# Kernel tuning notes

Hardware: AMD Instinct MI355X
Metric: run time of the kernel (lower is better)

Reference implementation:

```python
import jax, jax.numpy as jnp
import numpy as np

N, E, D, T = 100000, 1600000, 128, 5
EPS = 1e-5


def setup_inputs() -> dict:
    key = jax.random.key(0)
    ks = jax.random.split(key, 8)
    scale = 1.0 / np.sqrt(D)
    return {
        "features": jax.random.normal(ks[0], (N, D), dtype=jnp.float32),
        "src": jax.random.randint(ks[1], (E,), 0, N, dtype=jnp.int32),
        "dst": jax.random.randint(ks[2], (E,), 0, N, dtype=jnp.int32),
        "etype": jax.random.randint(ks[3], (E,), 0, T, dtype=jnp.int32),
        "w1": jax.random.normal(ks[4], (T * D, D), dtype=jnp.float32) * scale,
        "b1": jnp.zeros((T * D,), dtype=jnp.float32),
        "g1": jnp.ones((D,), dtype=jnp.float32),
        "be1": jnp.zeros((D,), dtype=jnp.float32),
        "w2": jax.random.normal(ks[5], (T * D, D), dtype=jnp.float32) * scale,
        "b2": jnp.zeros((T * D,), dtype=jnp.float32),
        "g2": jnp.ones((D,), dtype=jnp.float32),
        "be2": jnp.zeros((D,), dtype=jnp.float32),
    }


def _bn(x, gamma, beta):
    # BatchNorm1d in training mode: biased batch statistics over node axis.
    mu = jnp.mean(x, axis=0)
    var = jnp.mean((x - mu) ** 2, axis=0)
    return gamma * (x - mu) * jax.lax.rsqrt(var + EPS) + beta


def _round(x, w, b, gamma, beta, src, dst, etype):
    h = jax.nn.relu(_bn(x, gamma, beta))
    h = jnp.einsum('nd,od->no', h, w) + b          # [N, T*D]
    h3 = h.reshape(N, T, D)
    # one-hot multiply + sum over types == select the etype slice per edge
    msg = h3[src, etype]                            # [E, D] gather
    return jax.ops.segment_sum(msg, dst, num_segments=N)  # [N, D] scatter-add


def reference(features, src, dst, etype, w1, b1, g1, be1, w2, b2, g2, be2):
    h_new = _round(features, w1, b1, g1, be1, src, dst, etype)
    h_new = _round(h_new, w2, b2, g2, be2, src, dst, etype)
    return h_new + features
```

## Files before the change

### kernel.cpp

```cpp
#include <hip/hip_runtime.h>

#define NN 100000
#define EE 1600000
#define DD 128
#define TD 640
#define EPSV 1e-5f
#define NBLK_SCAN 391
#define SB 1024
#define NRANGE 8
#define RSZ 12500
#define NCHUNK 256
#define CSZ 6250

typedef __attribute__((ext_vector_type(8))) short bf16x8;
typedef __attribute__((ext_vector_type(4))) float f32x4;

__device__ inline unsigned short f2b(float f) {
  union { float f; unsigned u; } x; x.f = f;
  unsigned r = x.u + 0x7fff + ((x.u >> 16) & 1);
  return (unsigned short)(r >> 16);
}
__device__ inline float b2f(unsigned short u) {
  union { unsigned u; float f; } x; x.u = ((unsigned)u) << 16;
  return x.f;
}

__global__ __launch_bounds__(256) void k_stats_partial(const float* __restrict__ x,
    float* __restrict__ ps, float* __restrict__ pq) {
  float s0=0.f,s1=0.f,s2=0.f,s3=0.f,q0=0.f,q1=0.f,q2=0.f,q3=0.f;
  const float4* x4 = reinterpret_cast<const float4*>(x);
  const int total = NN * DD / 4;
  for (int i = blockIdx.x * 256 + threadIdx.x; i < total; i += SB * 256) {
    float4 v = x4[i];
    s0 += v.x; s1 += v.y; s2 += v.z; s3 += v.w;
    q0 += v.x*v.x; q1 += v.y*v.y; q2 += v.z*v.z; q3 += v.w*v.w;
  }
  __shared__ float ls[256], lq[256];
  int t = threadIdx.x;
  float sv[4] = {s0,s1,s2,s3}, qv[4] = {q0,q1,q2,q3};
#pragma unroll
  for (int j = 0; j < 4; ++j) {
    ls[t] = sv[j]; lq[t] = qv[j];
    __syncthreads();
    if (t < 32) {
      float a = 0.f, b = 0.f;
#pragma unroll
      for (int k = 0; k < 8; ++k) { a += ls[t + 32*k]; b += lq[t + 32*k]; }
      ps[blockIdx.x * DD + t*4 + j] = a;
      pq[blockIdx.x * DD + t*4 + j] = b;
    }
    __syncthreads();
  }
}

__global__ __launch_bounds__(256) void k_stats_partial_bf(const unsigned short* __restrict__ x,
    float* __restrict__ ps, float* __restrict__ pq) {
  float s0=0.f,s1=0.f,s2=0.f,s3=0.f,q0=0.f,q1=0.f,q2=0.f,q3=0.f;
  const ushort4* x4 = reinterpret_cast<const ushort4*>(x);
  const int total = NN * DD / 4;
  for (int i = blockIdx.x * 256 + threadIdx.x; i < total; i += SB * 256) {
    ushort4 u = x4[i];
    float vx = b2f(u.x), vy = b2f(u.y), vz = b2f(u.z), vw = b2f(u.w);
    s0 += vx; s1 += vy; s2 += vz; s3 += vw;
    q0 += vx*vx; q1 += vy*vy; q2 += vz*vz; q3 += vw*vw;
  }
  __shared__ float ls[256], lq[256];
  int t = threadIdx.x;
  float sv[4] = {s0,s1,s2,s3}, qv[4] = {q0,q1,q2,q3};
#pragma unroll
  for (int j = 0; j < 4; ++j) {
    ls[t] = sv[j]; lq[t] = qv[j];
    __syncthreads();
    if (t < 32) {
      float a = 0.f, b = 0.f;
#pragma unroll
      for (int k = 0; k < 8; ++k) { a += ls[t + 32*k]; b += lq[t + 32*k]; }
      ps[blockIdx.x * DD + t*4 + j] = a;
      pq[blockIdx.x * DD + t*4 + j] = b;
    }
    __syncthreads();
  }
}

__global__ __launch_bounds__(1024) void k_stats_final(const float* __restrict__ ps,
    const float* __restrict__ pq, const float* __restrict__ g,
    const float* __restrict__ be, float* __restrict__ ssb) {
  __shared__ float ls[1024], lq[1024];
  int t = threadIdx.x;
  int col = t & 127, seg = t >> 7;
  float s = 0.f, q = 0.f;
  for (int b = seg; b < SB; b += 8) { s += ps[b * DD + col]; q += pq[b * DD + col]; }
  ls[t] = s; lq[t] = q;
  __syncthreads();
  if (t < 128) {
#pragma unroll
    for (int k = 1; k < 8; ++k) { s += ls[t + 128*k]; q += lq[t + 128*k]; }
    float mean = s * (1.0f / NN);
    float var  = q * (1.0f / NN) - mean * mean;
    float sc = g[t] * rsqrtf(var + EPSV);
    ssb[t] = sc;
    ssb[DD + t] = be[t] - mean * sc;
  }
}

__global__ __launch_bounds__(256) void k_act(const float* __restrict__ x,
    const float* __restrict__ ss, unsigned short* __restrict__ A) {
  int i = blockIdx.x * 256 + threadIdx.x;
  float4 v = reinterpret_cast<const float4*>(x)[i];
  int c4 = (i & 31) * 4;
  float s0 = ss[c4+0], s1 = ss[c4+1], s2 = ss[c4+2], s3 = ss[c4+3];
  float h0 = ss[DD+c4+0], h1 = ss[DD+c4+1], h2 = ss[DD+c4+2], h3 = ss[DD+c4+3];
  ushort4 o;
  o.x = f2b(fmaxf(0.f, v.x * s0 + h0));
  o.y = f2b(fmaxf(0.f, v.y * s1 + h1));
  o.z = f2b(fmaxf(0.f, v.z * s2 + h2));
  o.w = f2b(fmaxf(0.f, v.w * s3 + h3));
  reinterpret_cast<ushort4*>(A)[i] = o;
}

__global__ __launch_bounds__(256) void k_act_bf(const unsigned short* __restrict__ x,
    const float* __restrict__ ss, unsigned short* __restrict__ A) {
  int i = blockIdx.x * 256 + threadIdx.x;
  ushort4 u = reinterpret_cast<const ushort4*>(x)[i];
  int c4 = (i & 31) * 4;
  float s0 = ss[c4+0], s1 = ss[c4+1], s2 = ss[c4+2], s3 = ss[c4+3];
  float h0 = ss[DD+c4+0], h1 = ss[DD+c4+1], h2 = ss[DD+c4+2], h3 = ss[DD+c4+3];
  ushort4 o;
  o.x = f2b(fmaxf(0.f, b2f(u.x) * s0 + h0));
  o.y = f2b(fmaxf(0.f, b2f(u.y) * s1 + h1));
  o.z = f2b(fmaxf(0.f, b2f(u.z) * s2 + h2));
  o.w = f2b(fmaxf(0.f, b2f(u.w) * s3 + h3));
  reinterpret_cast<ushort4*>(A)[i] = o;
}

__global__ void k_cvt_b2(const float* __restrict__ w, unsigned short* __restrict__ o) {
  int i = blockIdx.x * 256 + threadIdx.x;
  int tt = i >> 12;
  int rem = i & 4095;
  int d = rem >> 5, j = rem & 31;
  float4 v = reinterpret_cast<const float4*>(w)[i];
  ushort4 u; u.x = f2b(v.x); u.y = f2b(v.y); u.z = f2b(v.z); u.w = f2b(v.w);
  reinterpret_cast<ushort4*>(o)[d * 160 + tt * 32 + j] = u;
}

__global__ void k_zero(int* p, int n) {
  int i = blockIdx.x * 256 + threadIdx.x;
  if (i < n) p[i] = 0;
}
__global__ __launch_bounds__(256) void k_hist(const int* __restrict__ dst,
    int* __restrict__ cnt) {
  const int range = blockIdx.x & (NRANGE - 1);
  const int chunk = blockIdx.x >> 3;
  const int lo = range * RSZ;
  const int base = chunk * CSZ;
  for (int i = base + threadIdx.x; i < base + CSZ; i += 256) {
    int d = dst[i];
    if ((unsigned)(d - lo) < RSZ) atomicAdd(&cnt[d], 1);
  }
}
__global__ __launch_bounds__(256) void k_scan_blk(const int* __restrict__ cnt, int* __restrict__ bsum) {
  __shared__ int sh[256];
  int idx = blockIdx.x * 256 + threadIdx.x;
  sh[threadIdx.x] = (idx < NN) ? cnt[idx] : 0;
  __syncthreads();
  for (int off = 128; off > 0; off >>= 1) {
    if (threadIdx.x < off) sh[threadIdx.x] += sh[threadIdx.x + off];
    __syncthreads();
  }
  if (threadIdx.x == 0) bsum[blockIdx.x] = sh[0];
}
__global__ __launch_bounds__(512) void k_scan_top(int* __restrict__ bsum) {
  __shared__ int sh[512];
  int t = threadIdx.x;
  int v = (t < NBLK_SCAN) ? bsum[t] : 0;
  sh[t] = v;
  __syncthreads();
  for (int off = 1; off < 512; off <<= 1) {
    int add = (t >= off) ? sh[t - off] : 0;
    __syncthreads();
    sh[t] += add;
    __syncthreads();
  }
  if (t < NBLK_SCAN) bsum[t] = sh[t] - v;
}
__global__ __launch_bounds__(256) void k_scan_fin(const int* __restrict__ cnt,
    const int* __restrict__ bsum, int* __restrict__ row_ptr, int* __restrict__ cursor) {
  __shared__ int sh[256];
  int idx = blockIdx.x * 256 + threadIdx.x;
  int v = (idx < NN) ? cnt[idx] : 0;
  sh[threadIdx.x] = v;
  __syncthreads();
  for (int off = 1; off < 256; off <<= 1) {
    int add = (threadIdx.x >= off) ? sh[threadIdx.x - off] : 0;
    __syncthreads();
    sh[threadIdx.x] += add;
    __syncthreads();
  }
  int excl = bsum[blockIdx.x] + sh[threadIdx.x] - v;
  if (idx < NN) { row_ptr[idx] = excl; cursor[idx] = excl; }
  if (idx == NN - 1) row_ptr[NN] = excl + v;
}
__global__ __launch_bounds__(256) void k_scatter(const int* __restrict__ src,
    const int* __restrict__ dst, const int* __restrict__ et,
    int* __restrict__ cursor, int* __restrict__ payload) {
  const int range = blockIdx.x & (NRANGE - 1);
  const int chunk = blockIdx.x >> 3;
  const int lo = range * RSZ;
  const int base = chunk * CSZ;
  for (int i = base + threadIdx.x; i < base + CSZ; i += 256) {
    int d = dst[i];
    if ((unsigned)(d - lo) < RSZ) {
      int pos = atomicAdd(&cursor[d], 1);
      payload[pos] = (src[i] << 3) | et[i];
    }
  }
}

__global__ __launch_bounds__(256) void k_agg(const unsigned short* __restrict__ Ab,
    const int* __restrict__ rp, const int* __restrict__ pl,
    unsigned short* __restrict__ G, int* __restrict__ cntb) {
  const int n = blockIdx.x * 4 + (threadIdx.x >> 6);
  const int l = threadIdx.x & 63;
  const int s = rp[n], e = rp[n + 1];
  float a00=0.f,a01=0.f,a10=0.f,a11=0.f,a20=0.f,a21=0.f,a30=0.f,a31=0.f,a40=0.f,a41=0.f;
  int c0=0,c1=0,c2=0,c3=0,c4=0;
  int j = s;
  for (; j + 1 < e; j += 2) {
    int p0 = pl[j], p1 = pl[j + 1];
    ushort2 u0 = *reinterpret_cast<const ushort2*>(Ab + (p0 >> 3) * DD + 2 * l);
    ushort2 u1 = *reinterpret_cast<const ushort2*>(Ab + (p1 >> 3) * DD + 2 * l);
    float x0 = b2f(u0.x), x1 = b2f(u0.y);
    switch (p0 & 7) {
      case 0: a00 += x0; a01 += x1; c0++; break;
      case 1: a10 += x0; a11 += x1; c1++; break;
      case 2: a20 += x0; a21 += x1; c2++; break;
      case 3: a30 += x0; a31 += x1; c3++; break;
      default: a40 += x0; a41 += x1; c4++; break;
    }
    float z0 = b2f(u1.x), z1 = b2f(u1.y);
    switch (p1 & 7) {
      case 0: a00 += z0; a01 += z1; c0++; break;
      case 1: a10 += z0; a11 += z1; c1++; break;
      case 2: a20 += z0; a21 += z1; c2++; break;
      case 3: a30 += z0; a31 += z1; c3++; break;
      default: a40 += z0; a41 += z1; c4++; break;
    }
  }
  if (j < e) {
    int p0 = pl[j];
    ushort2 u0 = *reinterpret_cast<const ushort2*>(Ab + (p0 >> 3) * DD + 2 * l);
    float x0 = b2f(u0.x), x1 = b2f(u0.y);
    switch (p0 & 7) {
      case 0: a00 += x0; a01 += x1; c0++; break;
      case 1: a10 += x0; a11 += x1; c1++; break;
      case 2: a20 += x0; a21 += x1; c2++; break;
      case 3: a30 += x0; a31 += x1; c3++; break;
      default: a40 += x0; a41 += x1; c4++; break;
    }
  }
  unsigned short* gp = G + n * TD + 2 * l;
  ushort2 o;
  o.x = f2b(a00); o.y = f2b(a01); *reinterpret_cast<ushort2*>(gp + 0 * DD) = o;
  o.x = f2b(a10); o.y = f2b(a11); *reinterpret_cast<ushort2*>(gp + 1 * DD) = o;
  o.x = f2b(a20); o.y = f2b(a21); *reinterpret_cast<ushort2*>(gp + 2 * DD) = o;
  o.x = f2b(a30); o.y = f2b(a31); *reinterpret_cast<ushort2*>(gp + 3 * DD) = o;
  o.x = f2b(a40); o.y = f2b(a41); *reinterpret_cast<ushort2*>(gp + 4 * DD) = o;
  if (l < 5) {
    int c = (l == 0) ? c0 : (l == 1) ? c1 : (l == 2) ? c2 : (l == 3) ? c3 : c4;
    cntb[n * 8 + l] = c;
  }
}

template<int RND>
__global__ __launch_bounds__(256) void k_gemm2(const unsigned short* __restrict__ G,
    const unsigned short* __restrict__ B2, const float* __restrict__ bias,
    const int* __restrict__ cntb, const float* __restrict__ base,
    void* __restrict__ out) {
  __shared__ unsigned short wlds[2][8192];
  const int t = threadIdx.x;
  const int l = t & 63;
  const int w = t >> 6;
  const int lm = l & 15;
  const int hi = l >> 4;
  const int R = blockIdx.x * 64 + w * 16;

  int arow = R + lm; if (arow >= NN) arow = NN - 1;
  const unsigned short* aptr = G + arow * TD + hi * 8;

#pragma unroll
  for (int k = 0; k < 4; ++k) {
    int idx = k * 256 + t;
    int c = idx >> 3, sub = idx & 7;
    float4 v = *reinterpret_cast<const float4*>(
        reinterpret_cast<const char*>(B2) + c * 1280 + sub * 16);
    *reinterpret_cast<float4*>(
        reinterpret_cast<char*>(wlds[0]) + c * 128 + ((sub * 16) ^ ((c & 7) << 4))) = v;
  }
  __syncthreads();

  f32x4 acc[8] = {};
#pragma unroll 1
  for (int ks = 0; ks < 10; ++ks) {
    const int buf = ks & 1;
    if (ks < 9) {
#pragma unroll
      for (int k = 0; k < 4; ++k) {
        int idx = k * 256 + t;
        int c = idx >> 3, sub = idx & 7;
        float4 v = *reinterpret_cast<const float4*>(
            reinterpret_cast<const char*>(B2) + c * 1280 + (ks + 1) * 128 + sub * 16);
        *reinterpret_cast<float4*>(
            reinterpret_cast<char*>(wlds[buf ^ 1]) + c * 128 + ((sub * 16) ^ ((c & 7) << 4))) = v;
      }
    }
    bf16x8 af0 = *reinterpret_cast<const bf16x8*>(aptr + ks * 64);
    bf16x8 af1 = *reinterpret_cast<const bf16x8*>(aptr + ks * 64 + 32);
#pragma unroll
    for (int f = 0; f < 8; ++f) {
      int rr = f * 16 + lm;
      bf16x8 b0 = *reinterpret_cast<const bf16x8*>(
          reinterpret_cast<char*>(wlds[buf]) + rr * 128 + ((hi * 16) ^ ((rr & 7) << 4)));
      bf16x8 b1 = *reinterpret_cast<const bf16x8*>(
          reinterpret_cast<char*>(wlds[buf]) + rr * 128 + ((64 + hi * 16) ^ ((rr & 7) << 4)));
      acc[f] = __builtin_amdgcn_mfma_f32_16x16x32_bf16(af0, b0, acc[f], 0, 0, 0);
      acc[f] = __builtin_amdgcn_mfma_f32_16x16x32_bf16(af1, b1, acc[f], 0, 0, 0);
    }
    __syncthreads();
  }

  const int r0 = R + hi * 4;
  float cn[4][5];
#pragma unroll
  for (int r = 0; r < 4; ++r) {
    int row = r0 + r; if (row >= NN) row = NN - 1;
#pragma unroll
    for (int tt = 0; tt < 5; ++tt) cn[r][tt] = (float)cntb[row * 8 + tt];
  }
#pragma unroll
  for (int f = 0; f < 8; ++f) {
    int col = f * 16 + lm;
    float bb0 = bias[col], bb1 = bias[128 + col], bb2 = bias[256 + col],
          bb3 = bias[384 + col], bb4 = bias[512 + col];
#pragma unroll
    for (int r = 0; r < 4; ++r) {
      int row = r0 + r;
      if (row < NN) {
        float v = acc[f][r] + cn[r][0]*bb0 + cn[r][1]*bb1 + cn[r][2]*bb2
                            + cn[r][3]*bb3 + cn[r][4]*bb4;
        if (RND == 1) {
          v += base[row * DD + col];
          reinterpret_cast<float*>(out)[row * DD + col] = v;
        } else {
          reinterpret_cast<unsigned short*>(out)[row * DD + col] = f2b(v);
        }
      }
    }
  }
}

extern "C" void kernel_launch(void* const* d_in, const int* in_sizes, int n_in,
                              void* d_out, int out_size, void* d_ws, size_t ws_size,
                              hipStream_t stream) {
  const float* features = (const float*)d_in[0];
  const int*   src   = (const int*)d_in[1];
  const int*   dst   = (const int*)d_in[2];
  const int*   etype = (const int*)d_in[3];
  const float* w1  = (const float*)d_in[4];
  const float* b1  = (const float*)d_in[5];
  const float* g1  = (const float*)d_in[6];
  const float* be1 = (const float*)d_in[7];
  const float* w2  = (const float*)d_in[8];
  const float* b2  = (const float*)d_in[9];
  const float* g2  = (const float*)d_in[10];
  const float* be2 = (const float*)d_in[11];

  char* ws = (char*)d_ws;
  unsigned short* Ab   = (unsigned short*)(ws + 0);
  float*          ps   = (float*)(ws + 0);
  float*          pq   = (float*)(ws + 524288);
  unsigned short* G    = (unsigned short*)(ws + 25600000);
  unsigned short* y1   = (unsigned short*)(ws + 153600000);
  unsigned short* b2a  = (unsigned short*)(ws + 179200000);
  unsigned short* b2b  = (unsigned short*)(ws + 179363840);
  float*          ssb  = (float*)(ws + 179527680);
  int*            rowp = (int*)(ws + 179528704);
  int*            curs = (int*)(ws + 179928720);
  int*            payl = (int*)(ws + 180328720);
  int*            bsum = (int*)(ws + 186728720);
  int*            cntb = (int*)(ws + 186730768);

  k_zero<<<(NN + 255) / 256, 256, 0, stream>>>(curs, NN);
  k_hist<<<NRANGE * NCHUNK, 256, 0, stream>>>(dst, curs);
  k_scan_blk<<<NBLK_SCAN, 256, 0, stream>>>(curs, bsum);
  k_scan_top<<<1, 512, 0, stream>>>(bsum);
  k_scan_fin<<<NBLK_SCAN, 256, 0, stream>>>(curs, bsum, rowp, curs);
  k_scatter<<<NRANGE * NCHUNK, 256, 0, stream>>>(src, dst, etype, curs, payl);

  k_cvt_b2<<<80, 256, 0, stream>>>(w1, b2a);
  k_cvt_b2<<<80, 256, 0, stream>>>(w2, b2b);

  k_stats_partial<<<SB, 256, 0, stream>>>(features, ps, pq);
  k_stats_final<<<1, 1024, 0, stream>>>(ps, pq, g1, be1, ssb);
  k_act<<<12500, 256, 0, stream>>>(features, ssb, Ab);
  k_agg<<<NN / 4, 256, 0, stream>>>(Ab, rowp, payl, G, cntb);
  k_gemm2<0><<<1563, 256, 0, stream>>>(G, b2a, b1, cntb, nullptr, y1);

  k_stats_partial_bf<<<SB, 256, 0, stream>>>(y1, ps, pq);
  k_stats_final<<<1, 1024, 0, stream>>>(ps, pq, g2, be2, ssb);
  k_act_bf<<<12500, 256, 0, stream>>>(y1, ssb, Ab);
  k_agg<<<NN / 4, 256, 0, stream>>>(Ab, rowp, payl, G, cntb);
  k_gemm2<1><<<1563, 256, 0, stream>>>(G, b2b, b2, cntb, features, d_out);
}
```

Measured before the change: 610.7 us.

## Fuse per-type edge aggregation with the weight GEMM through shared memory

The per-node, per-type aggregation kernel and the MFMA GEMM kernel are merged into one kernel. Each 512-thread block aggregates 32 nodes into a swizzled shared-memory tile, then multiplies that tile by the weights with MFMA, reading B directly from global memory. This removes the 128MB bf16 intermediate G and the count buffer written to and re-read from HBM. In exchange, the weight matrix is re-read by every block without LDS staging, and the GEMM phase now waits on gather latency inside each block.

```diff
diff --git a/kernel.cpp b/kernel.cpp
--- a/kernel.cpp
+++ b/kernel.cpp
@@ -11,6 +11,7 @@
 #define RSZ 12500
 #define NCHUNK 256
 #define CSZ 6250
+#define FB 32
 
 typedef __attribute__((ext_vector_type(8))) short bf16x8;
 typedef __attribute__((ext_vector_type(4))) float f32x4;
@@ -216,144 +217,116 @@
   }
 }
 
-__global__ __launch_bounds__(256) void k_agg(const unsigned short* __restrict__ Ab,
+template<int RND>
+__global__ __launch_bounds__(512, 4) void k_fused(const unsigned short* __restrict__ Ab,
     const int* __restrict__ rp, const int* __restrict__ pl,
-    unsigned short* __restrict__ G, int* __restrict__ cntb) {
-  const int n = blockIdx.x * 4 + (threadIdx.x >> 6);
-  const int l = threadIdx.x & 63;
-  const int s = rp[n], e = rp[n + 1];
-  float a00=0.f,a01=0.f,a10=0.f,a11=0.f,a20=0.f,a21=0.f,a30=0.f,a31=0.f,a40=0.f,a41=0.f;
-  int c0=0,c1=0,c2=0,c3=0,c4=0;
-  int j = s;
-  for (; j + 1 < e; j += 2) {
-    int p0 = pl[j], p1 = pl[j + 1];
-    ushort2 u0 = *reinterpret_cast<const ushort2*>(Ab + (p0 >> 3) * DD + 2 * l);
-    ushort2 u1 = *reinterpret_cast<const ushort2*>(Ab + (p1 >> 3) * DD + 2 * l);
-    float x0 = b2f(u0.x), x1 = b2f(u0.y);
-    switch (p0 & 7) {
-      case 0: a00 += x0; a01 += x1; c0++; break;
-      case 1: a10 += x0; a11 += x1; c1++; break;
-      case 2: a20 += x0; a21 += x1; c2++; break;
-      case 3: a30 += x0; a31 += x1; c3++; break;
-      default: a40 += x0; a41 += x1; c4++; break;
-    }
-    float z0 = b2f(u1.x), z1 = b2f(u1.y);
-    switch (p1 & 7) {
-      case 0: a00 += z0; a01 += z1; c0++; break;
-      case 1: a10 += z0; a11 += z1; c1++; break;
-      case 2: a20 += z0; a21 += z1; c2++; break;
-      case 3: a30 += z0; a31 += z1; c3++; break;
-      default: a40 += z0; a41 += z1; c4++; break;
-    }
-  }
-  if (j < e) {
-    int p0 = pl[j];
-    ushort2 u0 = *reinterpret_cast<const ushort2*>(Ab + (p0 >> 3) * DD + 2 * l);
-    float x0 = b2f(u0.x), x1 = b2f(u0.y);
-    switch (p0 & 7) {
-      case 0: a00 += x0; a01 += x1; c0++; break;
-      case 1: a10 += x0; a11 += x1; c1++; break;
-      case 2: a20 += x0; a21 += x1; c2++; break;
-      case 3: a30 += x0; a31 += x1; c3++; break;
-      default: a40 += x0; a41 += x1; c4++; break;
-    }
-  }
-  unsigned short* gp = G + n * TD + 2 * l;
-  ushort2 o;
-  o.x = f2b(a00); o.y = f2b(a01); *reinterpret_cast<ushort2*>(gp + 0 * DD) = o;
-  o.x = f2b(a10); o.y = f2b(a11); *reinterpret_cast<ushort2*>(gp + 1 * DD) = o;
-  o.x = f2b(a20); o.y = f2b(a21); *reinterpret_cast<ushort2*>(gp + 2 * DD) = o;
-  o.x = f2b(a30); o.y = f2b(a31); *reinterpret_cast<ushort2*>(gp + 3 * DD) = o;
-  o.x = f2b(a40); o.y = f2b(a41); *reinterpret_cast<ushort2*>(gp + 4 * DD) = o;
-  if (l < 5) {
-    int c = (l == 0) ? c0 : (l == 1) ? c1 : (l == 2) ? c2 : (l == 3) ? c3 : c4;
-    cntb[n * 8 + l] = c;
-  }
-}
-
-template<int RND>
-__global__ __launch_bounds__(256) void k_gemm2(const unsigned short* __restrict__ G,
     const unsigned short* __restrict__ B2, const float* __restrict__ bias,
-    const int* __restrict__ cntb, const float* __restrict__ base,
-    void* __restrict__ out) {
-  __shared__ unsigned short wlds[2][8192];
+    const float* __restrict__ base, void* __restrict__ out) {
+  __shared__ __align__(16) unsigned short gl[FB * TD];
+  __shared__ int lcnt[FB][8];
   const int t = threadIdx.x;
   const int l = t & 63;
   const int w = t >> 6;
-  const int lm = l & 15;
-  const int hi = l >> 4;
-  const int R = blockIdx.x * 64 + w * 16;
-
-  int arow = R + lm; if (arow >= NN) arow = NN - 1;
-  const unsigned short* aptr = G + arow * TD + hi * 8;
-
-#pragma unroll
-  for (int k = 0; k < 4; ++k) {
-    int idx = k * 256 + t;
-    int c = idx >> 3, sub = idx & 7;
-    float4 v = *reinterpret_cast<const float4*>(
-        reinterpret_cast<const char*>(B2) + c * 1280 + sub * 16);
-    *reinterpret_cast<float4*>(
-        reinterpret_cast<char*>(wlds[0]) + c * 128 + ((sub * 16) ^ ((c & 7) << 4))) = v;
-  }
-  __syncthreads();
-
-  f32x4 acc[8] = {};
+  const int node0 = blockIdx.x * FB;
+  char* glc = reinterpret_cast<char*>(gl);
+
 #pragma unroll 1
-  for (int ks = 0; ks < 10; ++ks) {
-    const int buf = ks & 1;
-    if (ks < 9) {
-#pragma unroll
-      for (int k = 0; k < 4; ++k) {
-        int idx = k * 256 + t;
-        int c = idx >> 3, sub = idx & 7;
-        float4 v = *reinterpret_cast<const float4*>(
-            reinterpret_cast<const char*>(B2) + c * 1280 + (ks + 1) * 128 + sub * 16);
-        *reinterpret_cast<float4*>(
-            reinterpret_cast<char*>(wlds[buf ^ 1]) + c * 128 + ((sub * 16) ^ ((c & 7) << 4))) = v;
+  for (int i = 0; i < 4; ++i) {
+    const int nn = w * 4 + i;
+    const int n = node0 + nn;
+    const int s = rp[n], e = rp[n + 1];
+    float a00=0.f,a01=0.f,a10=0.f,a11=0.f,a20=0.f,a21=0.f,a30=0.f,a31=0.f,a40=0.f,a41=0.f;
+    int c0=0,c1=0,c2=0,c3=0,c4=0;
+    int j = s;
+    for (; j + 1 < e; j += 2) {
+      int p0 = pl[j], p1 = pl[j + 1];
+      ushort2 u0 = *reinterpret_cast<const ushort2*>(Ab + (p0 >> 3) * DD + 2 * l);
+      ushort2 u1 = *reinterpret_cast<const ushort2*>(Ab + (p1 >> 3) * DD + 2 * l);
+      float x0 = b2f(u0.x), x1 = b2f(u0.y);
+      switch (p0 & 7) {
+        case 0: a00 += x0; a01 += x1; c0++; break;
+        case 1: a10 += x0; a11 += x1; c1++; break;
+        case 2: a20 += x0; a21 += x1; c2++; break;
+        case 3: a30 += x0; a31 += x1; c3++; break;
+        default: a40 += x0; a41 += x1; c4++; break;
       }
-    }
-    bf16x8 af0 = *reinterpret_cast<const bf16x8*>(aptr + ks * 64);
-    bf16x8 af1 = *reinterpret_cast<const bf16x8*>(aptr + ks * 64 + 32);
-#pragma unroll
-    for (int f = 0; f < 8; ++f) {
-      int rr = f * 16 + lm;
-      bf16x8 b0 = *reinterpret_cast<const bf16x8*>(
-          reinterpret_cast<char*>(wlds[buf]) + rr * 128 + ((hi * 16) ^ ((rr & 7) << 4)));
-      bf16x8 b1 = *reinterpret_cast<const bf16x8*>(
-          reinterpret_cast<char*>(wlds[buf]) + rr * 128 + ((64 + hi * 16) ^ ((rr & 7) << 4)));
-      acc[f] = __builtin_amdgcn_mfma_f32_16x16x32_bf16(af0, b0, acc[f], 0, 0, 0);
-      acc[f] = __builtin_amdgcn_mfma_f32_16x16x32_bf16(af1, b1, acc[f], 0, 0, 0);
-    }
-    __syncthreads();
-  }
-
-  const int r0 = R + hi * 4;
-  float cn[4][5];
+      float z0 = b2f(u1.x), z1 = b2f(u1.y);
+      switch (p1 & 7) {
+        case 0: a00 += z0; a01 += z1; c0++; break;
+        case 1: a10 += z0; a11 += z1; c1++; break;
+        case 2: a20 += z0; a21 += z1; c2++; break;
+        case 3: a30 += z0; a31 += z1; c3++; break;
+        default: a40 += z0; a41 += z1; c4++; break;
+      }
+    }
+    if (j < e) {
+      int p0 = pl[j];
+      ushort2 u0 = *reinterpret_cast<const ushort2*>(Ab + (p0 >> 3) * DD + 2 * l);
+      float x0 = b2f(u0.x), x1 = b2f(u0.y);
+      switch (p0 & 7) {
+        case 0: a00 += x0; a01 += x1; c0++; break;
+        case 1: a10 += x0; a11 += x1; c1++; break;
+        case 2: a20 += x0; a21 += x1; c2++; break;
+        case 3: a30 += x0; a31 += x1; c3++; break;
+        default: a40 += x0; a41 += x1; c4++; break;
+      }
+    }
+    const unsigned rowbase = nn * (TD * 2);
+    const unsigned swz = (unsigned)((nn & 7) << 4);
+    ushort2 o;
+    o.x = f2b(a00); o.y = f2b(a01);
+    *reinterpret_cast<ushort2*>(glc + ((rowbase + 0*256 + 4*l) ^ swz)) = o;
+    o.x = f2b(a10); o.y = f2b(a11);
+    *reinterpret_cast<ushort2*>(glc + ((rowbase + 1*256 + 4*l) ^ swz)) = o;
+    o.x = f2b(a20); o.y = f2b(a21);
+    *reinterpret_cast<ushort2*>(glc + ((rowbase + 2*256 + 4*l) ^ swz)) = o;
+    o.x = f2b(a30); o.y = f2b(a31);
+    *reinterpret_cast<ushort2*>(glc + ((rowbase + 3*256 + 4*l) ^ swz)) = o;
+    o.x = f2b(a40); o.y = f2b(a41);
+    *reinterpret_cast<ushort2*>(glc + ((rowbase + 4*256 + 4*l) ^ swz)) = o;
+    if (l < 5) lcnt[nn][l] = (l == 0) ? c0 : (l == 1) ? c1 : (l == 2) ? c2 : (l == 3) ? c3 : c4;
+  }
+  __syncthreads();
+
+  const int rh = w >> 2;
+  const int wc = (w & 3) * 32;
+  const int lm = l & 15, hi = l >> 4;
+  const int rr = rh * 16 + lm;
+  const unsigned abase = (unsigned)(rr * (TD * 2));
+  const unsigned aswz = (unsigned)((rr & 7) << 4);
+  const unsigned short* bp0 = B2 + (wc + lm) * TD;
+  const unsigned short* bp1 = B2 + (wc + 16 + lm) * TD;
+  f32x4 acc0 = {}, acc1 = {};
+#pragma unroll 4
+  for (int kk = 0; kk < 20; ++kk) {
+    bf16x8 af = *reinterpret_cast<const bf16x8*>(glc + ((abase + kk*64 + hi*16) ^ aswz));
+    bf16x8 b0 = *reinterpret_cast<const bf16x8*>(bp0 + kk*32 + hi*8);
+    bf16x8 b1 = *reinterpret_cast<const bf16x8*>(bp1 + kk*32 + hi*8);
+    acc0 = __builtin_amdgcn_mfma_f32_16x16x32_bf16(af, b0, acc0, 0, 0, 0);
+    acc1 = __builtin_amdgcn_mfma_f32_16x16x32_bf16(af, b1, acc1, 0, 0, 0);
+  }
+
+  const int col0 = wc + lm, col1 = wc + 16 + lm;
+  float b00 = bias[col0], b01 = bias[128+col0], b02 = bias[256+col0],
+        b03 = bias[384+col0], b04 = bias[512+col0];
+  float b10 = bias[col1], b11 = bias[128+col1], b12 = bias[256+col1],
+        b13 = bias[384+col1], b14 = bias[512+col1];
 #pragma unroll
   for (int r = 0; r < 4; ++r) {
-    int row = r0 + r; if (row >= NN) row = NN - 1;
-#pragma unroll
-    for (int tt = 0; tt < 5; ++tt) cn[r][tt] = (float)cntb[row * 8 + tt];
-  }
-#pragma unroll
-  for (int f = 0; f < 8; ++f) {
-    int col = f * 16 + lm;
-    float bb0 = bias[col], bb1 = bias[128 + col], bb2 = bias[256 + col],
-          bb3 = bias[384 + col], bb4 = bias[512 + col];
-#pragma unroll
-    for (int r = 0; r < 4; ++r) {
-      int row = r0 + r;
-      if (row < NN) {
-        float v = acc[f][r] + cn[r][0]*bb0 + cn[r][1]*bb1 + cn[r][2]*bb2
-                            + cn[r][3]*bb3 + cn[r][4]*bb4;
-        if (RND == 1) {
-          v += base[row * DD + col];
-          reinterpret_cast<float*>(out)[row * DD + col] = v;
-        } else {
-          reinterpret_cast<unsigned short*>(out)[row * DD + col] = f2b(v);
-        }
-      }
+    int row = rh * 16 + hi * 4 + r;
+    int g = node0 + row;
+    float c0 = (float)lcnt[row][0], c1 = (float)lcnt[row][1], c2 = (float)lcnt[row][2],
+          c3 = (float)lcnt[row][3], c4 = (float)lcnt[row][4];
+    float v0 = acc0[r] + c0*b00 + c1*b01 + c2*b02 + c3*b03 + c4*b04;
+    float v1 = acc1[r] + c0*b10 + c1*b11 + c2*b12 + c3*b13 + c4*b14;
+    if (RND == 1) {
+      v0 += base[g * DD + col0];
+      v1 += base[g * DD + col1];
+      reinterpret_cast<float*>(out)[g * DD + col0] = v0;
+      reinterpret_cast<float*>(out)[g * DD + col1] = v1;
+    } else {
+      reinterpret_cast<unsigned short*>(out)[g * DD + col0] = f2b(v0);
+      reinterpret_cast<unsigned short*>(out)[g * DD + col1] = f2b(v1);
     }
   }
 }
@@ -378,16 +351,14 @@
   unsigned short* Ab   = (unsigned short*)(ws + 0);
   float*          ps   = (float*)(ws + 0);
   float*          pq   = (float*)(ws + 524288);
-  unsigned short* G    = (unsigned short*)(ws + 25600000);
-  unsigned short* y1   = (unsigned short*)(ws + 153600000);
-  unsigned short* b2a  = (unsigned short*)(ws + 179200000);
-  unsigned short* b2b  = (unsigned short*)(ws + 179363840);
-  float*          ssb  = (float*)(ws + 179527680);
-  int*            rowp = (int*)(ws + 179528704);
-  int*            curs = (int*)(ws + 179928720);
-  int*            payl = (int*)(ws + 180328720);
-  int*            bsum = (int*)(ws + 186728720);
-  int*            cntb = (int*)(ws + 186730768);
+  unsigned short* y1   = (unsigned short*)(ws + 25600000);
+  unsigned short* b2a  = (unsigned short*)(ws + 51200000);
+  unsigned short* b2b  = (unsigned short*)(ws + 51363840);
+  float*          ssb  = (float*)(ws + 51527680);
+  int*            rowp = (int*)(ws + 51528704);
+  int*            curs = (int*)(ws + 51928720);
+  int*            payl = (int*)(ws + 52328720);
+  int*            bsum = (int*)(ws + 58728720);
 
   k_zero<<<(NN + 255) / 256, 256, 0, stream>>>(curs, NN);
   k_hist<<<NRANGE * NCHUNK, 256, 0, stream>>>(dst, curs);
@@ -402,12 +373,10 @@
   k_stats_partial<<<SB, 256, 0, stream>>>(features, ps, pq);
   k_stats_final<<<1, 1024, 0, stream>>>(ps, pq, g1, be1, ssb);
   k_act<<<12500, 256, 0, stream>>>(features, ssb, Ab);
-  k_agg<<<NN / 4, 256, 0, stream>>>(Ab, rowp, payl, G, cntb);
-  k_gemm2<0><<<1563, 256, 0, stream>>>(G, b2a, b1, cntb, nullptr, y1);
+  k_fused<0><<<NN / FB, 512, 0, stream>>>(Ab, rowp, payl, b2a, b1, nullptr, y1);
 
   k_stats_partial_bf<<<SB, 256, 0, stream>>>(y1, ps, pq);
   k_stats_final<<<1, 1024, 0, stream>>>(ps, pq, g2, be2, ssb);
   k_act_bf<<<12500, 256, 0, stream>>>(y1, ssb, Ab);
-  k_agg<<<NN / 4, 256, 0, stream>>>(Ab, rowp, payl, G, cntb);
-  k_gemm2<1><<<1563, 256, 0, stream>>>(G, b2b, b2, cntb, features, d_out);
-}
+  k_fused<1><<<NN / FB, 512, 0, stream>>>(Ab, rowp, payl, b2b, b2, features, d_out);
+}
```

After: 772.7 us. 26.5% more time.

## Rework gemm2 to register-held weight tiles without LDS, unroll aggregation by four

Applied to the files above, without the earlier changes.

The second GEMM drops its LDS double-buffered weight staging and barriers. Each of 8 waves now owns 16 output columns, keeps its weight fragments in registers and reads A fragments for 4 row tiles straight from global memory, with 512-thread blocks. The aggregation loop is unrolled from two to four edges so more gathers are in flight. This removes LDS traffic and syncs but makes every wave reload the A rows from global/L2, and it raises register pressure.

```diff
diff --git a/kernel.cpp b/kernel.cpp
--- a/kernel.cpp
+++ b/kernel.cpp
@@ -225,39 +225,29 @@
   float a00=0.f,a01=0.f,a10=0.f,a11=0.f,a20=0.f,a21=0.f,a30=0.f,a31=0.f,a40=0.f,a41=0.f;
   int c0=0,c1=0,c2=0,c3=0,c4=0;
   int j = s;
-  for (; j + 1 < e; j += 2) {
-    int p0 = pl[j], p1 = pl[j + 1];
+#define ACC_ONE(P, U) do {                                              \
+    float x0 = b2f((U).x), x1 = b2f((U).y);                             \
+    switch ((P) & 7) {                                                  \
+      case 0: a00 += x0; a01 += x1; c0++; break;                        \
+      case 1: a10 += x0; a11 += x1; c1++; break;                        \
+      case 2: a20 += x0; a21 += x1; c2++; break;                        \
+      case 3: a30 += x0; a31 += x1; c3++; break;                        \
+      default: a40 += x0; a41 += x1; c4++; break;                       \
+    } } while (0)
+  for (; j + 3 < e; j += 4) {
+    int p0 = pl[j], p1 = pl[j + 1], p2 = pl[j + 2], p3 = pl[j + 3];
     ushort2 u0 = *reinterpret_cast<const ushort2*>(Ab + (p0 >> 3) * DD + 2 * l);
     ushort2 u1 = *reinterpret_cast<const ushort2*>(Ab + (p1 >> 3) * DD + 2 * l);
-    float x0 = b2f(u0.x), x1 = b2f(u0.y);
-    switch (p0 & 7) {
-      case 0: a00 += x0; a01 += x1; c0++; break;
-      case 1: a10 += x0; a11 += x1; c1++; break;
-      case 2: a20 += x0; a21 += x1; c2++; break;
-      case 3: a30 += x0; a31 += x1; c3++; break;
-      default: a40 += x0; a41 += x1; c4++; break;
-    }
-    float z0 = b2f(u1.x), z1 = b2f(u1.y);
-    switch (p1 & 7) {
-      case 0: a00 += z0; a01 += z1; c0++; break;
-      case 1: a10 += z0; a11 += z1; c1++; break;
-      case 2: a20 += z0; a21 += z1; c2++; break;
-      case 3: a30 += z0; a31 += z1; c3++; break;
-      default: a40 += z0; a41 += z1; c4++; break;
-    }
-  }
-  if (j < e) {
+    ushort2 u2 = *reinterpret_cast<const ushort2*>(Ab + (p2 >> 3) * DD + 2 * l);
+    ushort2 u3 = *reinterpret_cast<const ushort2*>(Ab + (p3 >> 3) * DD + 2 * l);
+    ACC_ONE(p0, u0); ACC_ONE(p1, u1); ACC_ONE(p2, u2); ACC_ONE(p3, u3);
+  }
+  for (; j < e; ++j) {
     int p0 = pl[j];
     ushort2 u0 = *reinterpret_cast<const ushort2*>(Ab + (p0 >> 3) * DD + 2 * l);
-    float x0 = b2f(u0.x), x1 = b2f(u0.y);
-    switch (p0 & 7) {
-      case 0: a00 += x0; a01 += x1; c0++; break;
-      case 1: a10 += x0; a11 += x1; c1++; break;
-      case 2: a20 += x0; a21 += x1; c2++; break;
-      case 3: a30 += x0; a31 += x1; c3++; break;
-      default: a40 += x0; a41 += x1; c4++; break;
-    }
-  }
+    ACC_ONE(p0, u0);
+  }
+#undef ACC_ONE
   unsigned short* gp = G + n * TD + 2 * l;
   ushort2 o;
   o.x = f2b(a00); o.y = f2b(a01); *reinterpret_cast<ushort2*>(gp + 0 * DD) = o;
@@ -272,81 +262,50 @@
 }
 
 template<int RND>
-__global__ __launch_bounds__(256) void k_gemm2(const unsigned short* __restrict__ G,
+__global__ __launch_bounds__(512, 4) void k_gemm2(const unsigned short* __restrict__ G,
     const unsigned short* __restrict__ B2, const float* __restrict__ bias,
     const int* __restrict__ cntb, const float* __restrict__ base,
     void* __restrict__ out) {
-  __shared__ unsigned short wlds[2][8192];
   const int t = threadIdx.x;
   const int l = t & 63;
   const int w = t >> 6;
-  const int lm = l & 15;
-  const int hi = l >> 4;
-  const int R = blockIdx.x * 64 + w * 16;
-
-  int arow = R + lm; if (arow >= NN) arow = NN - 1;
-  const unsigned short* aptr = G + arow * TD + hi * 8;
-
-#pragma unroll
-  for (int k = 0; k < 4; ++k) {
-    int idx = k * 256 + t;
-    int c = idx >> 3, sub = idx & 7;
-    float4 v = *reinterpret_cast<const float4*>(
-        reinterpret_cast<const char*>(B2) + c * 1280 + sub * 16);
-    *reinterpret_cast<float4*>(
-        reinterpret_cast<char*>(wlds[0]) + c * 128 + ((sub * 16) ^ ((c & 7) << 4))) = v;
-  }
-  __syncthreads();
-
-  f32x4 acc[8] = {};
-#pragma unroll 1
-  for (int ks = 0; ks < 10; ++ks) {
-    const int buf = ks & 1;
-    if (ks < 9) {
-#pragma unroll
-      for (int k = 0; k < 4; ++k) {
-        int idx = k * 256 + t;
-        int c = idx >> 3, sub = idx & 7;
-        float4 v = *reinterpret_cast<const float4*>(
-            reinterpret_cast<const char*>(B2) + c * 1280 + (ks + 1) * 128 + sub * 16);
-        *reinterpret_cast<float4*>(
-            reinterpret_cast<char*>(wlds[buf ^ 1]) + c * 128 + ((sub * 16) ^ ((c & 7) << 4))) = v;
+  const int lm = l & 15, hi = l >> 4;
+  const int col = w * 16 + lm;
+  const int R = blockIdx.x * 64;
+
+  const unsigned short* bp = B2 + col * TD + hi * 8;
+  const unsigned short* ap[4];
+#pragma unroll
+  for (int rt = 0; rt < 4; ++rt) {
+    int ar = R + rt * 16 + lm; if (ar >= NN) ar = NN - 1;
+    ap[rt] = G + ar * TD + hi * 8;
+  }
+  f32x4 acc[4] = {};
+#pragma unroll
+  for (int kb = 0; kb < 4; ++kb) {
+    bf16x8 bfr[5];
+#pragma unroll
+    for (int k5 = 0; k5 < 5; ++k5)
+      bfr[k5] = *reinterpret_cast<const bf16x8*>(bp + (kb * 5 + k5) * 32);
+#pragma unroll
+    for (int k5 = 0; k5 < 5; ++k5) {
+#pragma unroll
+      for (int rt = 0; rt < 4; ++rt) {
+        bf16x8 af = *reinterpret_cast<const bf16x8*>(ap[rt] + (kb * 5 + k5) * 32);
+        acc[rt] = __builtin_amdgcn_mfma_f32_16x16x32_bf16(af, bfr[k5], acc[rt], 0, 0, 0);
       }
     }
-    bf16x8 af0 = *reinterpret_cast<const bf16x8*>(aptr + ks * 64);
-    bf16x8 af1 = *reinterpret_cast<const bf16x8*>(aptr + ks * 64 + 32);
-#pragma unroll
-    for (int f = 0; f < 8; ++f) {
-      int rr = f * 16 + lm;
-      bf16x8 b0 = *reinterpret_cast<const bf16x8*>(
-          reinterpret_cast<char*>(wlds[buf]) + rr * 128 + ((hi * 16) ^ ((rr & 7) << 4)));
-      bf16x8 b1 = *reinterpret_cast<const bf16x8*>(
-          reinterpret_cast<char*>(wlds[buf]) + rr * 128 + ((64 + hi * 16) ^ ((rr & 7) << 4)));
-      acc[f] = __builtin_amdgcn_mfma_f32_16x16x32_bf16(af0, b0, acc[f], 0, 0, 0);
-      acc[f] = __builtin_amdgcn_mfma_f32_16x16x32_bf16(af1, b1, acc[f], 0, 0, 0);
-    }
-    __syncthreads();
-  }
-
-  const int r0 = R + hi * 4;
-  float cn[4][5];
-#pragma unroll
-  for (int r = 0; r < 4; ++r) {
-    int row = r0 + r; if (row >= NN) row = NN - 1;
-#pragma unroll
-    for (int tt = 0; tt < 5; ++tt) cn[r][tt] = (float)cntb[row * 8 + tt];
-  }
-#pragma unroll
-  for (int f = 0; f < 8; ++f) {
-    int col = f * 16 + lm;
-    float bb0 = bias[col], bb1 = bias[128 + col], bb2 = bias[256 + col],
-          bb3 = bias[384 + col], bb4 = bias[512 + col];
+  }
+  float bb0 = bias[col], bb1 = bias[128 + col], bb2 = bias[256 + col],
+        bb3 = bias[384 + col], bb4 = bias[512 + col];
+#pragma unroll
+  for (int rt = 0; rt < 4; ++rt) {
 #pragma unroll
     for (int r = 0; r < 4; ++r) {
-      int row = r0 + r;
+      int row = R + rt * 16 + hi * 4 + r;
       if (row < NN) {
-        float v = acc[f][r] + cn[r][0]*bb0 + cn[r][1]*bb1 + cn[r][2]*bb2
-                            + cn[r][3]*bb3 + cn[r][4]*bb4;
+        const int* cp = cntb + row * 8;
+        float v = acc[rt][r] + cp[0]*bb0 + cp[1]*bb1 + cp[2]*bb2 + cp[3]*bb3 + cp[4]*bb4;
         if (RND == 1) {
           v += base[row * DD + col];
           reinterpret_cast<float*>(out)[row * DD + col] = v;
@@ -403,11 +362,11 @@
   k_stats_final<<<1, 1024, 0, stream>>>(ps, pq, g1, be1, ssb);
   k_act<<<12500, 256, 0, stream>>>(features, ssb, Ab);
   k_agg<<<NN / 4, 256, 0, stream>>>(Ab, rowp, payl, G, cntb);
-  k_gemm2<0><<<1563, 256, 0, stream>>>(G, b2a, b1, cntb, nullptr, y1);
+  k_gemm2<0><<<1563, 512, 0, stream>>>(G, b2a, b1, cntb, nullptr, y1);
 
   k_stats_partial_bf<<<SB, 256, 0, stream>>>(y1, ps, pq);
   k_stats_final<<<1, 1024, 0, stream>>>(ps, pq, g2, be2, ssb);
   k_act_bf<<<12500, 256, 0, stream>>>(y1, ssb, Ab);
   k_agg<<<NN / 4, 256, 0, stream>>>(Ab, rowp, payl, G, cntb);
-  k_gemm2<1><<<1563, 256, 0, stream>>>(G, b2b, b2, cntb, features, d_out);
-}
+  k_gemm2<1><<<1563, 512, 0, stream>>>(G, b2b, b2, cntb, features, d_out);
+}
```

Measured after the change: 793.4 us. 1.3x slower.

## Stage A tile through LDS with register-prefetched double buffering in gemm2

Applied to the files above, without the earlier changes.

Reworks the second GEMM kernel so both the A tile (gathered rows of G) and the B weight tile go through global-to-register prefetch for the next K step, are written to swizzled double-buffered LDS after compute, and are then read from LDS for the MFMA fragments. Previously A fragments were loaded straight from global memory with strided per-lane loads. This aims to coalesce A loads and hide their latency behind compute, and adds an occupancy hint of 3 blocks. The cost is more LDS, an extra barrier per K step, and count values now read per row inside the epilogue instead of being cached.

```diff
diff --git a/kernel.cpp b/kernel.cpp
--- a/kernel.cpp
+++ b/kernel.cpp
@@ -272,81 +272,83 @@
 }
 
 template<int RND>
-__global__ __launch_bounds__(256) void k_gemm2(const unsigned short* __restrict__ G,
+__global__ __launch_bounds__(256, 3) void k_gemm2(const unsigned short* __restrict__ G,
     const unsigned short* __restrict__ B2, const float* __restrict__ bias,
     const int* __restrict__ cntb, const float* __restrict__ base,
     void* __restrict__ out) {
-  __shared__ unsigned short wlds[2][8192];
+  __shared__ __align__(16) unsigned short alds[2][4096];
+  __shared__ __align__(16) unsigned short blds[2][8192];
   const int t = threadIdx.x;
   const int l = t & 63;
   const int w = t >> 6;
-  const int lm = l & 15;
-  const int hi = l >> 4;
-  const int R = blockIdx.x * 64 + w * 16;
-
-  int arow = R + lm; if (arow >= NN) arow = NN - 1;
-  const unsigned short* aptr = G + arow * TD + hi * 8;
-
-#pragma unroll
-  for (int k = 0; k < 4; ++k) {
-    int idx = k * 256 + t;
-    int c = idx >> 3, sub = idx & 7;
-    float4 v = *reinterpret_cast<const float4*>(
-        reinterpret_cast<const char*>(B2) + c * 1280 + sub * 16);
-    *reinterpret_cast<float4*>(
-        reinterpret_cast<char*>(wlds[0]) + c * 128 + ((sub * 16) ^ ((c & 7) << 4))) = v;
-  }
+  const int lm = l & 15, hi = l >> 4;
+  const int R = blockIdx.x * 64;
+  const int trow = t >> 3;
+  const int slot = t & 7;
+
+  float4 areg[2], breg[4];
+
+#define LOADREGS(KS) do {                                                      \
+  _Pragma("unroll") for (int it = 0; it < 2; ++it) {                           \
+    int row = it * 32 + trow; int ar = R + row; if (ar >= NN) ar = NN - 1;     \
+    areg[it] = *reinterpret_cast<const float4*>(G + ar * TD + (KS) * 64 + slot * 8); } \
+  _Pragma("unroll") for (int it = 0; it < 4; ++it) {                           \
+    int col = it * 32 + trow;                                                  \
+    breg[it] = *reinterpret_cast<const float4*>(B2 + col * TD + (KS) * 64 + slot * 8); } \
+} while (0)
+
+#define WRITELDS(BUF) do {                                                     \
+  char* ac_ = (char*)alds[BUF]; char* bc_ = (char*)blds[BUF];                  \
+  _Pragma("unroll") for (int it = 0; it < 2; ++it) {                           \
+    int row = it * 32 + trow;                                                  \
+    *reinterpret_cast<float4*>(ac_ + row * 128 + ((slot * 16) ^ ((row & 7) << 4))) = areg[it]; } \
+  _Pragma("unroll") for (int it = 0; it < 4; ++it) {                           \
+    int col = it * 32 + trow;                                                  \
+    *reinterpret_cast<float4*>(bc_ + col * 128 + ((slot * 16) ^ ((col & 7) << 4))) = breg[it]; } \
+} while (0)
+
+  f32x4 acc[8] = {};
+  const int rowA = w * 16 + lm;
+  const unsigned sw = (unsigned)((lm & 7) << 4);
+
+  LOADREGS(0);
+  WRITELDS(0);
   __syncthreads();
-
-  f32x4 acc[8] = {};
 #pragma unroll 1
   for (int ks = 0; ks < 10; ++ks) {
     const int buf = ks & 1;
-    if (ks < 9) {
-#pragma unroll
-      for (int k = 0; k < 4; ++k) {
-        int idx = k * 256 + t;
-        int c = idx >> 3, sub = idx & 7;
-        float4 v = *reinterpret_cast<const float4*>(
-            reinterpret_cast<const char*>(B2) + c * 1280 + (ks + 1) * 128 + sub * 16);
-        *reinterpret_cast<float4*>(
-            reinterpret_cast<char*>(wlds[buf ^ 1]) + c * 128 + ((sub * 16) ^ ((c & 7) << 4))) = v;
-      }
-    }
-    bf16x8 af0 = *reinterpret_cast<const bf16x8*>(aptr + ks * 64);
-    bf16x8 af1 = *reinterpret_cast<const bf16x8*>(aptr + ks * 64 + 32);
-#pragma unroll
-    for (int f = 0; f < 8; ++f) {
-      int rr = f * 16 + lm;
-      bf16x8 b0 = *reinterpret_cast<const bf16x8*>(
-          reinterpret_cast<char*>(wlds[buf]) + rr * 128 + ((hi * 16) ^ ((rr & 7) << 4)));
-      bf16x8 b1 = *reinterpret_cast<const bf16x8*>(
-          reinterpret_cast<char*>(wlds[buf]) + rr * 128 + ((64 + hi * 16) ^ ((rr & 7) << 4)));
-      acc[f] = __builtin_amdgcn_mfma_f32_16x16x32_bf16(af0, b0, acc[f], 0, 0, 0);
-      acc[f] = __builtin_amdgcn_mfma_f32_16x16x32_bf16(af1, b1, acc[f], 0, 0, 0);
-    }
-    __syncthreads();
-  }
-
-  const int r0 = R + hi * 4;
-  float cn[4][5];
-#pragma unroll
-  for (int r = 0; r < 4; ++r) {
-    int row = r0 + r; if (row >= NN) row = NN - 1;
-#pragma unroll
-    for (int tt = 0; tt < 5; ++tt) cn[r][tt] = (float)cntb[row * 8 + tt];
-  }
-#pragma unroll
-  for (int f = 0; f < 8; ++f) {
-    int col = f * 16 + lm;
+    if (ks < 9) LOADREGS(ks + 1);
+    char* ac = (char*)alds[buf];
+    char* bc = (char*)blds[buf];
+    bf16x8 a0 = *reinterpret_cast<const bf16x8*>(ac + rowA * 128 + ((hi * 16) ^ sw));
+    bf16x8 a1 = *reinterpret_cast<const bf16x8*>(ac + rowA * 128 + ((64 + hi * 16) ^ sw));
+#pragma unroll
+    for (int cf = 0; cf < 8; ++cf) {
+      int colB = cf * 16 + lm;
+      bf16x8 b0 = *reinterpret_cast<const bf16x8*>(bc + colB * 128 + ((hi * 16) ^ sw));
+      bf16x8 b1 = *reinterpret_cast<const bf16x8*>(bc + colB * 128 + ((64 + hi * 16) ^ sw));
+      acc[cf] = __builtin_amdgcn_mfma_f32_16x16x32_bf16(a0, b0, acc[cf], 0, 0, 0);
+      acc[cf] = __builtin_amdgcn_mfma_f32_16x16x32_bf16(a1, b1, acc[cf], 0, 0, 0);
+    }
+    __syncthreads();
+    if (ks < 9) WRITELDS(buf ^ 1);
+    __syncthreads();
+  }
+#undef LOADREGS
+#undef WRITELDS
+
+  const int r0 = w * 16 + hi * 4;
+#pragma unroll
+  for (int cf = 0; cf < 8; ++cf) {
+    int col = cf * 16 + lm;
     float bb0 = bias[col], bb1 = bias[128 + col], bb2 = bias[256 + col],
           bb3 = bias[384 + col], bb4 = bias[512 + col];
 #pragma unroll
     for (int r = 0; r < 4; ++r) {
-      int row = r0 + r;
+      int row = R + r0 + r;
       if (row < NN) {
-        float v = acc[f][r] + cn[r][0]*bb0 + cn[r][1]*bb1 + cn[r][2]*bb2
-                            + cn[r][3]*bb3 + cn[r][4]*bb4;
+        const int* cp = cntb + row * 8;
+        float v = acc[cf][r] + cp[0]*bb0 + cp[1]*bb1 + cp[2]*bb2 + cp[3]*bb3 + cp[4]*bb4;
         if (RND == 1) {
           v += base[row * DD + col];
           reinterpret_cast<float*>(out)[row * DD + col] = v;
```

Result: slower. 784.6 us (+28.5%).
